# Kernel optimization log

Measured on AMD Instinct MI355X. Metric: run time of the kernel, lower is better.

Reference implementation:

```python
import jax, jax.numpy as jnp
import numpy as np

M, P, B, TLEN = 512, 256, 128, 1024

def setup_inputs() -> dict:
    key = jax.random.key(0)
    k1, k2, k3, k4, k5, k6 = jax.random.split(key, 6)
    d_t = jax.random.normal(k1, (1, B, P), dtype=jnp.float32)
    s_t = jax.random.normal(k2, (1, B, P), dtype=jnp.float32)
    H = jax.random.normal(k3, (B, TLEN, M), dtype=jnp.float32)
    # torch.nn.Linear weights: shape [out_features, in_features]
    W_d = jax.random.normal(k4, (M, 2 * P), dtype=jnp.float32) / np.sqrt(2 * P)
    U_d = jax.random.normal(k5, (M, M), dtype=jnp.float32) / np.sqrt(M)
    v_d = jax.random.normal(k6, (1, M), dtype=jnp.float32) / np.sqrt(M)
    return {"d_t": d_t, "s_t": s_t, "H": H, "T": TLEN, "W_d": W_d, "U_d": U_d, "v_d": v_d}

def reference(d_t, s_t, H, T, W_d, U_d, v_d):
    # query: cat([d_t, s_t], dim=2) -> [1, B, 2p]; permute(1,0,2) -> [B, 1, 2p]
    query = jnp.concatenate([d_t, s_t], axis=2).transpose(1, 0, 2)  # [B, 1, 2p]
    # W_d(query) broadcast over T instead of materializing the repeat (same math)
    wq = jnp.einsum('boc,mc->bom', query, W_d)          # [B, 1, m]
    uh = jnp.einsum('btm,nm->btn', H, U_d)              # [B, T, m]
    beta = jnp.tanh(wq + uh)                            # [B, T, m]
    score = jnp.einsum('btm,om->bto', beta, v_d)        # [B, T, 1]
    score = score.transpose(0, 2, 1)                    # [B, 1, T]
    return jax.nn.softmax(score, axis=2)
```

## Files before the change

### kernel.cpp

```cpp
#include <hip/hip_runtime.h>
#include <hip/hip_bf16.h>
#include <stdint.h>

#define NB   128
#define NT   1024
#define NM   512
#define NP   256

typedef __attribute__((ext_vector_type(8))) short bf16x8;
typedef __attribute__((ext_vector_type(4))) float f32x4;
typedef unsigned int u32;

__device__ __forceinline__ uint32_t bfpair(float a, float b) {
    uint32_t ua = __float_as_uint(a) + 0x8000u;
    uint32_t ub = __float_as_uint(b) + 0x8000u;
    return __builtin_amdgcn_perm(ub, ua, 0x07060302u);
}

__device__ __forceinline__ float fast_tanh(float x) {
    float e = __expf(2.0f * x);
    return 1.0f - 2.0f * __builtin_amdgcn_rcpf(e + 1.0f);
}

typedef const __attribute__((address_space(1))) u32* gas_t;
typedef __attribute__((address_space(3))) u32* las_t;
__device__ __forceinline__ void dma16(const void* g, void* l) {
    __builtin_amdgcn_global_load_lds((gas_t)g, (las_t)l, 16, 0, 0);
}

__global__ void prep_kernel(const float* __restrict__ U, unsigned short* __restrict__ Ub,
                            const float* __restrict__ d_t, const float* __restrict__ s_t,
                            const float* __restrict__ W, float* __restrict__ wq,
                            float* __restrict__ out) {
    const int bx = blockIdx.x;
    if (bx < 256) {
        int idx = bx * 256 + threadIdx.x;
        float4 u = reinterpret_cast<const float4*>(U)[idx];
        reinterpret_cast<uint2*>(Ub)[idx] = make_uint2(bfpair(u.x, u.y), bfpair(u.z, u.w));
    } else if (bx < 384) {
        int g = (bx - 256) * 512 + threadIdx.x * 2;
        int b = g >> 9;
        const float* dt = d_t + (size_t)b * NP;
        const float* st = s_t + (size_t)b * NP;
        #pragma unroll
        for (int e = 0; e < 2; ++e) {
            int n = (g + e) & 511;
            const float* Wn = W + (size_t)n * 512;
            float s = 0.f;
            #pragma unroll 4
            for (int c = 0; c < NP; c += 4) {
                float4 w0 = *reinterpret_cast<const float4*>(Wn + c);
                float4 q0 = *reinterpret_cast<const float4*>(dt + c);
                s += w0.x * q0.x + w0.y * q0.y + w0.z * q0.z + w0.w * q0.w;
                float4 w1 = *reinterpret_cast<const float4*>(Wn + NP + c);
                float4 q1 = *reinterpret_cast<const float4*>(st + c);
                s += w1.x * q1.x + w1.y * q1.y + w1.z * q1.z + w1.w * q1.w;
            }
            wq[g + e] = s;
        }
    } else {
        int idx = (bx - 384) * 256 + threadIdx.x;
        reinterpret_cast<float4*>(out)[idx] = make_float4(0.f, 0.f, 0.f, 0.f);
    }
}

__global__ __launch_bounds__(256, 2)
void score_kernel(const float* __restrict__ H, const unsigned short* __restrict__ Ub,
                  const float* __restrict__ wq, const float* __restrict__ v_d,
                  float* __restrict__ out) {
    __shared__ unsigned short As[2][128 * 32];
    __shared__ unsigned short Bs[3][256 * 32];
    __shared__ float s_score[128];

    const int tid  = threadIdx.x;
    const int id   = blockIdx.x;
    const int tile = (id >> 4) * 8 + (id & 7);
    const int nh   = (id >> 3) & 1;
    const int tt   = tile & 7;
    const int b    = tile >> 3;

    const int lane = tid & 63;
    const int w    = tid >> 6;
    const int lr   = lane & 15;
    const int lq   = lane >> 4;
    const int tw   = w >> 1;
    const int nw   = w & 1;

    if (tid < 128) s_score[tid] = 0.f;

    const float* gA[4];
    u32 woff[4];
    #pragma unroll
    for (int q = 0; q < 4; ++q) {
        int r = w * 32 + q * 8 + (lane >> 3);
        gA[q] = H + ((size_t)(b * NT + tt * 128 + r)) * NM + (lane & 7) * 4;
        woff[q] = (u32)(r * 64 + ((((lane & 7) >> 1) ^ ((r >> 1) & 3)) << 4) + (lane & 1) * 8);
    }
    const unsigned short* gB[4];
    u32 lB[4];
    #pragma unroll
    for (int q = 0; q < 4; ++q) {
        int rB = w * 64 + q * 16 + (lane >> 2);
        int cB = (lane & 3) ^ ((rB >> 1) & 3);
        gB[q] = Ub + ((size_t)(nh * 256 + rB)) * NM + cB * 8;
        lB[q] = (u32)((w * 4 + q) * 1024 + lane * 16);
    }
    const u32 aro = (u32)((tw * 64 + lr) * 64 + ((lq ^ ((lr >> 1) & 3)) << 4));
    const u32 bro = (u32)((nw * 128 + lr) * 64 + ((lq ^ ((lr >> 1) & 3)) << 4));

    f32x4 acc[4][8];
    #pragma unroll
    for (int i = 0; i < 4; ++i)
        #pragma unroll
        for (int j = 0; j < 8; ++j)
            acc[i][j] = (f32x4){0.f, 0.f, 0.f, 0.f};

    float4 av[4];
    #pragma unroll
    for (int q = 0; q < 4; ++q) { av[q] = *reinterpret_cast<const float4*>(gA[q]); gA[q] += 32; }
    #pragma unroll
    for (int q = 0; q < 4; ++q) { dma16(gB[q], (char*)Bs[0] + lB[q]); gB[q] += 32; }
    #pragma unroll
    for (int q = 0; q < 4; ++q)
        *reinterpret_cast<uint2*>((char*)As[0] + woff[q]) =
            make_uint2(bfpair(av[q].x, av[q].y), bfpair(av[q].z, av[q].w));
    #pragma unroll
    for (int q = 0; q < 4; ++q) { av[q] = *reinterpret_cast<const float4*>(gA[q]); gA[q] += 32; }
    #pragma unroll
    for (int q = 0; q < 4; ++q) { dma16(gB[q], (char*)Bs[1] + lB[q]); gB[q] += 32; }

    asm volatile("s_waitcnt vmcnt(8)" ::: "memory");
    asm volatile("s_waitcnt lgkmcnt(0)" ::: "memory");
    __builtin_amdgcn_s_barrier();
    __builtin_amdgcn_sched_barrier(0);

    #pragma unroll
    for (int kk = 0; kk < 16; ++kk) {
        const char* ab = (const char*)As[kk & 1] + aro;
        bf16x8 a0 = *reinterpret_cast<const bf16x8*>(ab);
        bf16x8 a1 = *reinterpret_cast<const bf16x8*>(ab + 1024);
        bf16x8 a2 = *reinterpret_cast<const bf16x8*>(ab + 2048);
        bf16x8 a3 = *reinterpret_cast<const bf16x8*>(ab + 3072);

        if (kk < 15) {
            char* an = (char*)As[(kk + 1) & 1];
            #pragma unroll
            for (int q = 0; q < 4; ++q)
                *reinterpret_cast<uint2*>(an + woff[q]) =
                    make_uint2(bfpair(av[q].x, av[q].y), bfpair(av[q].z, av[q].w));
        }
        if (kk < 14) {
            #pragma unroll
            for (int q = 0; q < 4; ++q) { av[q] = *reinterpret_cast<const float4*>(gA[q]); gA[q] += 32; }
            char* bn = (char*)Bs[(kk + 2) % 3];
            #pragma unroll
            for (int q = 0; q < 4; ++q) { dma16(gB[q], bn + lB[q]); gB[q] += 32; }
        }

        const char* bbb = (const char*)Bs[kk % 3] + bro;
        #pragma unroll
        for (int j = 0; j < 8; ++j) {
            bf16x8 bbj = *reinterpret_cast<const bf16x8*>(bbb + j * 1024);
            acc[0][j] = __builtin_amdgcn_mfma_f32_16x16x32_bf16(a0, bbj, acc[0][j], 0, 0, 0);
            acc[1][j] = __builtin_amdgcn_mfma_f32_16x16x32_bf16(a1, bbj, acc[1][j], 0, 0, 0);
            acc[2][j] = __builtin_amdgcn_mfma_f32_16x16x32_bf16(a2, bbj, acc[2][j], 0, 0, 0);
            acc[3][j] = __builtin_amdgcn_mfma_f32_16x16x32_bf16(a3, bbj, acc[3][j], 0, 0, 0);
        }

        if (kk < 14) {
            asm volatile("s_waitcnt vmcnt(8)" ::: "memory");
        } else if (kk == 14) {
            asm volatile("s_waitcnt vmcnt(0)" ::: "memory");
        }
        if (kk < 15) {
            asm volatile("s_waitcnt lgkmcnt(0)" ::: "memory");
            __builtin_amdgcn_s_barrier();
            __builtin_amdgcn_sched_barrier(0);
        }
    }

    const float* wqb = wq + (size_t)b * NM;
    float vv[8], wv[8];
    #pragma unroll
    for (int j = 0; j < 8; ++j) {
        int n = nh * 256 + nw * 128 + j * 16 + lr;
        vv[j] = v_d[n];
        wv[j] = wqb[n];
    }
    #pragma unroll
    for (int i = 0; i < 4; ++i) {
        #pragma unroll
        for (int r = 0; r < 4; ++r) {
            float s = 0.f;
            #pragma unroll
            for (int j = 0; j < 8; ++j)
                s += vv[j] * fast_tanh(wv[j] + acc[i][j][r]);
            #pragma unroll
            for (int off = 1; off < 16; off <<= 1)
                s += __shfl_xor(s, off, 64);
            if (lr == 0) atomicAdd(&s_score[tw * 64 + i * 16 + lq * 4 + r], s);
        }
    }
    __syncthreads();
    if (tid < 128) atomicAdd(&out[(size_t)b * NT + tt * 128 + tid], s_score[tid]);
}

__global__ void softmax_kernel(float* __restrict__ out) {
    const int b   = blockIdx.x;
    const int tid = threadIdx.x;
    float* p = out + (size_t)b * NT;
    float4 v = reinterpret_cast<float4*>(p)[tid];
    float m = fmaxf(fmaxf(v.x, v.y), fmaxf(v.z, v.w));
    #pragma unroll
    for (int off = 32; off >= 1; off >>= 1)
        m = fmaxf(m, __shfl_xor(m, off, 64));
    __shared__ float red[8];
    const int wv = tid >> 6;
    if ((tid & 63) == 0) red[wv] = m;
    __syncthreads();
    m = fmaxf(fmaxf(red[0], red[1]), fmaxf(red[2], red[3]));
    float e0 = __expf(v.x - m), e1 = __expf(v.y - m);
    float e2 = __expf(v.z - m), e3 = __expf(v.w - m);
    float s = e0 + e1 + e2 + e3;
    #pragma unroll
    for (int off = 32; off >= 1; off >>= 1)
        s += __shfl_xor(s, off, 64);
    if ((tid & 63) == 0) red[4 + wv] = s;
    __syncthreads();
    s = red[4] + red[5] + red[6] + red[7];
    float inv = 1.f / s;
    float4 o;
    o.x = e0 * inv; o.y = e1 * inv; o.z = e2 * inv; o.w = e3 * inv;
    reinterpret_cast<float4*>(p)[tid] = o;
}

extern "C" void kernel_launch(void* const* d_in, const int* in_sizes, int n_in,
                              void* d_out, int out_size, void* d_ws, size_t ws_size,
                              hipStream_t stream) {
    const float* d_t = (const float*)d_in[0];
    const float* s_t = (const float*)d_in[1];
    const float* H   = (const float*)d_in[2];
    const float* W_d = (const float*)d_in[4];
    const float* U_d = (const float*)d_in[5];
    const float* v_d = (const float*)d_in[6];
    float* out = (float*)d_out;

    unsigned short* Ub = (unsigned short*)d_ws;
    float* wq = (float*)((char*)d_ws + 512 * 1024);

    prep_kernel<<<512, 256, 0, stream>>>(U_d, Ub, d_t, s_t, W_d, wq, out);
    score_kernel<<<2048, 256, 0, stream>>>(H, Ub, wq, v_d, out);
    softmax_kernel<<<NB, 256, 0, stream>>>(out);
}
```

Measured before the change: 455.4 us.

## Double score-kernel block to 512 threads with smaller per-wave N tile

Each score block now runs 8 waves (2 along T, 4 along N), with each wave covering 64 columns instead of 128. This halves the accumulator registers per thread and the per-thread H/U load work. The k-loop is no longer unrolled and uses rotating LDS offsets, which shrinks code size. The A-tile conversion store is moved after the MFMAs so the H loads have more time to land. The aim is higher occupancy and better latency hiding, at the cost of more waves sharing the same LDS tiles, more barrier participants and loop overhead from the rolled loop.

Measured after the change: 464.0 us. No clear change (+1.9%).

```diff
diff --git a/kernel.cpp b/kernel.cpp
--- a/kernel.cpp
+++ b/kernel.cpp
@@ -64,7 +64,7 @@
     }
 }
 
-__global__ __launch_bounds__(256, 2)
+__global__ __launch_bounds__(512, 4)
 void score_kernel(const float* __restrict__ H, const unsigned short* __restrict__ Ub,
                   const float* __restrict__ wq, const float* __restrict__ v_d,
                   float* __restrict__ out) {
@@ -83,107 +83,110 @@
     const int w    = tid >> 6;
     const int lr   = lane & 15;
     const int lq   = lane >> 4;
-    const int tw   = w >> 1;
-    const int nw   = w & 1;
+    const int tw   = w >> 2;
+    const int nw   = w & 3;
 
     if (tid < 128) s_score[tid] = 0.f;
 
-    const float* gA[4];
-    u32 woff[4];
-    #pragma unroll
-    for (int q = 0; q < 4; ++q) {
-        int r = w * 32 + q * 8 + (lane >> 3);
-        gA[q] = H + ((size_t)(b * NT + tt * 128 + r)) * NM + (lane & 7) * 4;
-        woff[q] = (u32)(r * 64 + ((((lane & 7) >> 1) ^ ((r >> 1) & 3)) << 4) + (lane & 1) * 8);
-    }
-    const unsigned short* gB[4];
-    u32 lB[4];
-    #pragma unroll
-    for (int q = 0; q < 4; ++q) {
-        int rB = w * 64 + q * 16 + (lane >> 2);
-        int cB = (lane & 3) ^ ((rB >> 1) & 3);
-        gB[q] = Ub + ((size_t)(nh * 256 + rB)) * NM + cB * 8;
-        lB[q] = (u32)((w * 4 + q) * 1024 + lane * 16);
-    }
+    const int rA = tid >> 2, uA = tid & 3;
+    const float* gA = H + ((size_t)(b * NT + tt * 128 + rA)) * NM + uA * 8;
+    const u32 woff = (u32)(rA * 64 + ((uA ^ ((rA >> 1) & 3)) << 4));
+
+    const unsigned short* gB0, * gB1;
+    u32 lB0, lB1;
+    {
+        int rB0 = w * 32 + (lane >> 2);
+        int rB1 = rB0 + 16;
+        gB0 = Ub + ((size_t)(nh * 256 + rB0)) * NM + (((lane & 3) ^ ((rB0 >> 1) & 3)) * 8);
+        gB1 = Ub + ((size_t)(nh * 256 + rB1)) * NM + (((lane & 3) ^ ((rB1 >> 1) & 3)) * 8);
+        lB0 = (u32)((w * 32) * 64 + lane * 16);
+        lB1 = lB0 + 16 * 64;
+    }
+
     const u32 aro = (u32)((tw * 64 + lr) * 64 + ((lq ^ ((lr >> 1) & 3)) << 4));
-    const u32 bro = (u32)((nw * 128 + lr) * 64 + ((lq ^ ((lr >> 1) & 3)) << 4));
-
-    f32x4 acc[4][8];
+    const u32 bro = (u32)((nw * 64 + lr) * 64 + ((lq ^ ((lr >> 1) & 3)) << 4));
+
+    f32x4 acc[4][4];
     #pragma unroll
     for (int i = 0; i < 4; ++i)
         #pragma unroll
-        for (int j = 0; j < 8; ++j)
+        for (int j = 0; j < 4; ++j)
             acc[i][j] = (f32x4){0.f, 0.f, 0.f, 0.f};
 
-    float4 av[4];
-    #pragma unroll
-    for (int q = 0; q < 4; ++q) { av[q] = *reinterpret_cast<const float4*>(gA[q]); gA[q] += 32; }
-    #pragma unroll
-    for (int q = 0; q < 4; ++q) { dma16(gB[q], (char*)Bs[0] + lB[q]); gB[q] += 32; }
-    #pragma unroll
-    for (int q = 0; q < 4; ++q)
-        *reinterpret_cast<uint2*>((char*)As[0] + woff[q]) =
-            make_uint2(bfpair(av[q].x, av[q].y), bfpair(av[q].z, av[q].w));
-    #pragma unroll
-    for (int q = 0; q < 4; ++q) { av[q] = *reinterpret_cast<const float4*>(gA[q]); gA[q] += 32; }
-    #pragma unroll
-    for (int q = 0; q < 4; ++q) { dma16(gB[q], (char*)Bs[1] + lB[q]); gB[q] += 32; }
-
-    asm volatile("s_waitcnt vmcnt(8)" ::: "memory");
+    float4 av0 = *reinterpret_cast<const float4*>(gA);
+    float4 av1 = *reinterpret_cast<const float4*>(gA + 4);
+    gA += 32;
+    dma16(gB0, (char*)Bs[0] + lB0);
+    dma16(gB1, (char*)Bs[0] + lB1);
+    gB0 += 32; gB1 += 32;
+    dma16(gB0, (char*)Bs[1] + lB0);
+    dma16(gB1, (char*)Bs[1] + lB1);
+    gB0 += 32; gB1 += 32;
+    {
+        uint4 wv4;
+        wv4.x = bfpair(av0.x, av0.y); wv4.y = bfpair(av0.z, av0.w);
+        wv4.z = bfpair(av1.x, av1.y); wv4.w = bfpair(av1.z, av1.w);
+        *reinterpret_cast<uint4*>((char*)As[0] + woff) = wv4;
+    }
+    asm volatile("s_waitcnt vmcnt(2)" ::: "memory");
     asm volatile("s_waitcnt lgkmcnt(0)" ::: "memory");
     __builtin_amdgcn_s_barrier();
     __builtin_amdgcn_sched_barrier(0);
 
-    #pragma unroll
+    u32 offA = 0;
+    u32 rb0 = 0, rb1 = 16384, rb2 = 32768;
+
+    #pragma unroll 1
     for (int kk = 0; kk < 16; ++kk) {
-        const char* ab = (const char*)As[kk & 1] + aro;
+        const char* ab = (const char*)As + offA + aro;
         bf16x8 a0 = *reinterpret_cast<const bf16x8*>(ab);
         bf16x8 a1 = *reinterpret_cast<const bf16x8*>(ab + 1024);
         bf16x8 a2 = *reinterpret_cast<const bf16x8*>(ab + 2048);
         bf16x8 a3 = *reinterpret_cast<const bf16x8*>(ab + 3072);
 
+        float4 nv0, nv1;
         if (kk < 15) {
-            char* an = (char*)As[(kk + 1) & 1];
-            #pragma unroll
-            for (int q = 0; q < 4; ++q)
-                *reinterpret_cast<uint2*>(an + woff[q]) =
-                    make_uint2(bfpair(av[q].x, av[q].y), bfpair(av[q].z, av[q].w));
+            nv0 = *reinterpret_cast<const float4*>(gA);
+            nv1 = *reinterpret_cast<const float4*>(gA + 4);
+            gA += 32;
         }
         if (kk < 14) {
-            #pragma unroll
-            for (int q = 0; q < 4; ++q) { av[q] = *reinterpret_cast<const float4*>(gA[q]); gA[q] += 32; }
-            char* bn = (char*)Bs[(kk + 2) % 3];
-            #pragma unroll
-            for (int q = 0; q < 4; ++q) { dma16(gB[q], bn + lB[q]); gB[q] += 32; }
-        }
-
-        const char* bbb = (const char*)Bs[kk % 3] + bro;
-        #pragma unroll
-        for (int j = 0; j < 8; ++j) {
-            bf16x8 bbj = *reinterpret_cast<const bf16x8*>(bbb + j * 1024);
-            acc[0][j] = __builtin_amdgcn_mfma_f32_16x16x32_bf16(a0, bbj, acc[0][j], 0, 0, 0);
-            acc[1][j] = __builtin_amdgcn_mfma_f32_16x16x32_bf16(a1, bbj, acc[1][j], 0, 0, 0);
-            acc[2][j] = __builtin_amdgcn_mfma_f32_16x16x32_bf16(a2, bbj, acc[2][j], 0, 0, 0);
-            acc[3][j] = __builtin_amdgcn_mfma_f32_16x16x32_bf16(a3, bbj, acc[3][j], 0, 0, 0);
-        }
-
-        if (kk < 14) {
-            asm volatile("s_waitcnt vmcnt(8)" ::: "memory");
-        } else if (kk == 14) {
-            asm volatile("s_waitcnt vmcnt(0)" ::: "memory");
-        }
+            char* bwr = (char*)Bs + rb2;
+            dma16(gB0, bwr + lB0);
+            dma16(gB1, bwr + lB1);
+            gB0 += 32; gB1 += 32;
+        }
+
+        const char* bb = (const char*)Bs + rb0 + bro;
+        #pragma unroll
+        for (int j = 0; j < 4; ++j) {
+            bf16x8 bj = *reinterpret_cast<const bf16x8*>(bb + j * 1024);
+            acc[0][j] = __builtin_amdgcn_mfma_f32_16x16x32_bf16(a0, bj, acc[0][j], 0, 0, 0);
+            acc[1][j] = __builtin_amdgcn_mfma_f32_16x16x32_bf16(a1, bj, acc[1][j], 0, 0, 0);
+            acc[2][j] = __builtin_amdgcn_mfma_f32_16x16x32_bf16(a2, bj, acc[2][j], 0, 0, 0);
+            acc[3][j] = __builtin_amdgcn_mfma_f32_16x16x32_bf16(a3, bj, acc[3][j], 0, 0, 0);
+        }
+
         if (kk < 15) {
+            char* an = (char*)As + (offA ^ 8192) + woff;
+            uint4 wv4;
+            wv4.x = bfpair(nv0.x, nv0.y); wv4.y = bfpair(nv0.z, nv0.w);
+            wv4.z = bfpair(nv1.x, nv1.y); wv4.w = bfpair(nv1.z, nv1.w);
+            *reinterpret_cast<uint4*>(an) = wv4;
+            asm volatile("s_waitcnt vmcnt(2)" ::: "memory");
             asm volatile("s_waitcnt lgkmcnt(0)" ::: "memory");
             __builtin_amdgcn_s_barrier();
             __builtin_amdgcn_sched_barrier(0);
         }
+        offA ^= 8192;
+        u32 t = rb0; rb0 = rb1; rb1 = rb2; rb2 = t;
     }
 
     const float* wqb = wq + (size_t)b * NM;
-    float vv[8], wv[8];
-    #pragma unroll
-    for (int j = 0; j < 8; ++j) {
-        int n = nh * 256 + nw * 128 + j * 16 + lr;
+    float vv[4], wv[4];
+    #pragma unroll
+    for (int j = 0; j < 4; ++j) {
+        int n = nh * 256 + nw * 64 + j * 16 + lr;
         vv[j] = v_d[n];
         wv[j] = wqb[n];
     }
@@ -193,7 +196,7 @@
         for (int r = 0; r < 4; ++r) {
             float s = 0.f;
             #pragma unroll
-            for (int j = 0; j < 8; ++j)
+            for (int j = 0; j < 4; ++j)
                 s += vv[j] * fast_tanh(wv[j] + acc[i][j][r]);
             #pragma unroll
             for (int off = 1; off < 16; off <<= 1)
@@ -249,6 +252,6 @@
     float* wq = (float*)((char*)d_ws + 512 * 1024);
 
     prep_kernel<<<512, 256, 0, stream>>>(U_d, Ub, d_t, s_t, W_d, wq, out);
-    score_kernel<<<2048, 256, 0, stream>>>(H, Ub, wq, v_d, out);
+    score_kernel<<<2048, 512, 0, stream>>>(H, Ub, wq, v_d, out);
     softmax_kernel<<<NB, 256, 0, stream>>>(out);
 }
```
